# Optimization experiments

Measured on AMD Instinct MI355X. Metric: run time of the kernel, lower is better.

## Reference

```python
import jax, jax.numpy as jnp
import numpy as np

N_NODES = 100000
NUM_FEAT = 64
NUM_CLASS = 40
N_EDGES = 1600000


def setup_inputs() -> dict:
    key = jax.random.key(0)
    k1, k2, k3, k4, k5 = jax.random.split(key, 5)
    x = jax.random.normal(k1, (N_NODES, NUM_FEAT), dtype=jnp.float32)
    index = jax.random.randint(k2, (2, N_EDGES), 0, N_NODES, dtype=jnp.int64)
    # SAGEConv params: lin_l applied to aggregated neighbors (has bias),
    # lin_r applied to root features (no bias) -- PyG convention.
    s = 1.0 / np.sqrt(NUM_FEAT)
    lin_l_w = jax.random.uniform(k3, (NUM_FEAT, NUM_CLASS), dtype=jnp.float32, minval=-s, maxval=s)
    lin_l_b = jnp.zeros((NUM_CLASS,), dtype=jnp.float32)
    lin_r_w = jax.random.uniform(k4, (NUM_FEAT, NUM_CLASS), dtype=jnp.float32, minval=-s, maxval=s)
    return {"x": x, "index": index, "lin_l_w": lin_l_w, "lin_l_b": lin_l_b, "lin_r_w": lin_r_w}


def reference(x, index, lin_l_w, lin_l_b, lin_r_w):
    src, dst = index[0], index[1]
    # Mean aggregation over incoming neighbors: messages flow src -> dst.
    msg = x[src]                                        # [E, F] gather
    agg_sum = jax.ops.segment_sum(msg, dst, num_segments=N_NODES)   # [N, F]
    deg = jax.ops.segment_sum(jnp.ones((index.shape[1],), dtype=x.dtype), dst,
                              num_segments=N_NODES)     # [N]
    agg = agg_sum / jnp.maximum(deg, 1.0)[:, None]      # mean, safe for isolated nodes
    out = agg @ lin_l_w + lin_l_b + x @ lin_r_w         # [N, C]
    return jax.nn.log_softmax(out, axis=1)
```

## Files before the change

kernel.cpp:

```cpp
#include <hip/hip_runtime.h>
#include <hip/hip_fp8.h>
#include <math.h>

constexpr int NODES = 100000;
constexpr int F = 64;
constexpr int C = 40;
constexpr int NPB   = 128;
constexpr int NB    = (NODES + NPB - 1) / NPB;
constexpr int NBPAD = 1024;
constexpr int BCAP  = 2816;
constexpr int TILE  = 4096;
constexpr int NTILES = NODES / 16;
constexpr int MBLK  = (NTILES + 3) / 4;

typedef __attribute__((ext_vector_type(8))) short short8;
typedef __attribute__((ext_vector_type(4))) float floatx4;
typedef __attribute__((ext_vector_type(2))) float floatx2;

__device__ inline unsigned bf16pack2(float a, float b) {
    unsigned ua = __builtin_bit_cast(unsigned, a);
    unsigned ub = __builtin_bit_cast(unsigned, b);
    ua += 0x7FFFu + ((ua >> 16) & 1u);
    ub += 0x7FFFu + ((ub >> 16) & 1u);
    return (ua >> 16) | (ub & 0xFFFF0000u);
}
__device__ inline unsigned short bf16of(float a) {
    unsigned ua = __builtin_bit_cast(unsigned, a);
    ua += 0x7FFFu + ((ua >> 16) & 1u);
    return (unsigned short)(ua >> 16);
}
__device__ inline float bf16tof(unsigned short u) {
    return __builtin_bit_cast(float, (unsigned)u << 16);
}
__device__ inline unsigned char fp8of(float f) {
    __hip_fp8_e4m3 q(f);
    return (unsigned char)q.__x;
}
template <int K>
__device__ inline float fp8byte(unsigned d) {
    __hip_fp8_e4m3 v;
    v.__x = (__hip_fp8_storage_t)((d >> (8 * K)) & 0xFFu);
    return (float)v;
}
template <int HI>
__device__ inline floatx2 fp8pk(unsigned d) {
#if __has_builtin(__builtin_amdgcn_cvt_pk_f32_fp8)
    return __builtin_amdgcn_cvt_pk_f32_fp8((int)d, HI != 0);
#else
    floatx2 r;
    r[0] = fp8byte<HI ? 2 : 0>(d);
    r[1] = fp8byte<HI ? 3 : 1>(d);
    return r;
#endif
}

__global__ __launch_bounds__(256)
void fused_A(const float* __restrict__ x,
             const float* __restrict__ wl,
             const float* __restrict__ bl,
             const float* __restrict__ wr,
             const int* __restrict__ src, const int* __restrict__ dst,
             int* __restrict__ gcursor, int* __restrict__ bbuf, int nedges,
             unsigned char* __restrict__ y8f, unsigned short* __restrict__ z8) {
    __shared__ union {
        struct { int lhist[NB]; int lcur[NB]; } bz;
        struct { unsigned sB[10 * 64 * 4]; float sbl[40]; } mf;
    } sh;

    int t = threadIdx.x;

    if (blockIdx.x < MBLK) {
        if (t < 40) sh.mf.sbl[t] = bl[t];
        for (int s = t; s < 640; s += 256) {
            int region = s >> 6;
            int l      = s & 63;
            int ct = region >> 1, ks = region & 1;
            int col = ct * 16 + (l & 15);
            int fb  = ks * 32 + ((l >> 4) << 3);
            const float* wsrc = (col < 40) ? (wl + col) : (wr + (col - 40));
            unsigned* dstp = &sh.mf.sB[s * 4];
#pragma unroll
            for (int p = 0; p < 4; ++p) {
                float a = wsrc[(fb + 2 * p) * 40];
                float b = wsrc[(fb + 2 * p + 1) * 40];
                dstp[p] = bf16pack2(a, b);
            }
        }
        __syncthreads();

        int lane = t & 63;
        int nt = blockIdx.x * 4 + (t >> 6);
        if (nt >= NTILES) return;

        union U { unsigned u[4]; short8 v; };
        short8 bf[5][2];
#pragma unroll
        for (int ct = 0; ct < 5; ++ct)
#pragma unroll
            for (int ks = 0; ks < 2; ++ks) {
                U tmp;
                const uint4* p =
                    (const uint4*)&sh.mf.sB[((ct * 2 + ks) * 64 + lane) * 4];
                uint4 q = *p;
                tmp.u[0] = q.x; tmp.u[1] = q.y; tmp.u[2] = q.z; tmp.u[3] = q.w;
                bf[ct][ks] = tmp.v;
            }

        floatx4 acc[5];
#pragma unroll
        for (int ct = 0; ct < 5; ++ct) {
            int col = ct * 16 + (lane & 15);
            float bias = (col >= 40) ? sh.mf.sbl[col - 40] : 0.0f;
            acc[ct] = (floatx4){bias, bias, bias, bias};
        }

        int row = nt * 16 + (lane & 15);
        const float4* xp = (const float4*)(x + (size_t)row * F);
        short8 af[2];
#pragma unroll
        for (int ks = 0; ks < 2; ++ks) {
            int kb = ks * 8 + ((lane >> 4) << 1);
            float4 va = xp[kb];
            float4 vb = xp[kb + 1];
            U a;
            a.u[0] = bf16pack2(va.x, va.y);
            a.u[1] = bf16pack2(va.z, va.w);
            a.u[2] = bf16pack2(vb.x, vb.y);
            a.u[3] = bf16pack2(vb.z, vb.w);
            af[ks] = a.v;
        }

#pragma unroll
        for (int ks = 0; ks < 2; ++ks)
#pragma unroll
            for (int ct = 0; ct < 5; ++ct)
                acc[ct] = __builtin_amdgcn_mfma_f32_16x16x32_bf16(
                    af[ks], bf[ct][ks], acc[ct], 0, 0, 0);

#pragma unroll
        for (int ct = 0; ct < 5; ++ct) {
            int col = ct * 16 + (lane & 15);
#pragma unroll
            for (int r = 0; r < 4; ++r) {
                int grow = nt * 16 + ((lane >> 4) << 2) + r;
                if (col < 40) y8f[(size_t)grow * C + col]       = fp8of(acc[ct][r]);
                else          z8[(size_t)grow * C + (col - 40)] = bf16of(acc[ct][r]);
            }
        }
    } else {
        for (int i = t; i < NB; i += 256) sh.bz.lhist[i] = 0;
        __syncthreads();

        int bb = blockIdx.x - MBLK;
        int base = bb * TILE;
        int pk[16], bk[16];
#pragma unroll
        for (int u = 0; u < 16; ++u) {
            int e = base + u * 256 + t;
            bk[u] = -1;
            if (e < nedges) {
                int s = src[e], d = dst[e];
                if ((unsigned)s < (unsigned)NODES && (unsigned)d < (unsigned)NODES) {
                    bk[u] = d >> 7;
                    pk[u] = s | ((d & 127) << 17);
                    atomicAdd(&sh.bz.lhist[bk[u]], 1);
                }
            }
        }
        __syncthreads();
        for (int i = t; i < NB; i += 256) {
            int c = sh.bz.lhist[i];
            sh.bz.lcur[i] = c ? atomicAdd(&gcursor[i], c) : 0;
        }
        __syncthreads();
#pragma unroll
        for (int u = 0; u < 16; ++u) {
            if (bk[u] >= 0) {
                int p = atomicAdd(&sh.bz.lcur[bk[u]], 1);
                if (p < BCAP) bbuf[(size_t)bk[u] * BCAP + p] = pk[u];
            }
        }
    }
}

__global__ __launch_bounds__(256)
void local_sort(const int* __restrict__ bbuf, const int* __restrict__ gcount,
                int* __restrict__ sorted_src, int* __restrict__ off,
                int* __restrict__ deg) {
    __shared__ int lhist[NPB];
    __shared__ int lcur[NPB];
    __shared__ int wred[4];
    __shared__ int w0tot;

    int b = blockIdx.x;
    int t = threadIdx.x;
    int lane = t & 63, wv = t >> 6;

    int part = 0;
    for (int i = t; i < b; i += 256) part += gcount[i];
#pragma unroll
    for (int d = 1; d < 64; d <<= 1) part += __shfl_xor(part, d);
    if (lane == 0) wred[wv] = part;
    if (t < NPB) lhist[t] = 0;
    __syncthreads();
    int ebase = wred[0] + wred[1] + wred[2] + wred[3];

    int cnt = gcount[b];
    if (cnt > BCAP) cnt = BCAP;
    const int* myb = bbuf + (size_t)b * BCAP;

    for (int i = t; i < cnt; i += 256)
        atomicAdd(&lhist[myb[i] >> 17], 1);
    __syncthreads();

    int c = 0, sc = 0;
    if (t < NPB) {
        c = lhist[t];
        sc = c;
#pragma unroll
        for (int d = 1; d < 64; d <<= 1) {
            int o = __shfl_up(sc, d);
            if (lane >= d) sc += o;
        }
    }
    if (t == 63) w0tot = sc;
    __syncthreads();
    if (t >= 64 && t < NPB) sc += w0tot;
    if (t < NPB) {
        int excl = ebase + sc - c;
        lcur[t] = excl;
        int n = b * NPB + t;
        if (n < NODES) { off[n] = excl; deg[n] = c; }
    }
    __syncthreads();

    for (int i = t; i < cnt; i += 256) {
        int pk = myb[i];
        int p = atomicAdd(&lcur[pk >> 17], 1);
        sorted_src[p] = pk & 0x1FFFF;
    }
}

__global__ __launch_bounds__(256)
void aggregate_v4(const unsigned char* __restrict__ y8f,
                  const unsigned short* __restrict__ z8,
                  const int* __restrict__ sorted_src,
                  const int* __restrict__ off,
                  const int* __restrict__ deg,
                  float* __restrict__ out) {
    int t = threadIdx.x;
    int lane = t & 63;
    int n = blockIdx.x * 4 + (t >> 6);
    if (n >= NODES) return;

    int g = lane >> 3;
    int i = lane & 7;
    bool valid = (i < 5);
    int byteoff = (valid ? i : 4) * 8;

    int base = __builtin_amdgcn_readfirstlane(off[n]);
    int cnt  = __builtin_amdgcn_readfirstlane(deg[n]);

    int li = lane < cnt ? lane : (cnt > 0 ? cnt - 1 : 0);
    int idxv = sorted_src[base + li];

    uint4 zv = make_uint4(0u, 0u, 0u, 0u);
    if (valid) zv = *(const uint4*)(z8 + (size_t)n * C + i * 8);

    unsigned d0[8], d1[8];
#pragma unroll
    for (int k = 0; k < 8; ++k) { d0[k] = 0u; d1[k] = 0u; }
#pragma unroll
    for (int k = 0; k < 8; ++k) {
        if (cnt > 8 * k) {
            int s = __shfl(idxv, 8 * k + g);
            const unsigned* p = (const unsigned*)(y8f + (size_t)s * C + byteoff);
            d0[k] = p[0];
            d1[k] = p[1];
        }
    }

    float acc[8] = {0.f, 0.f, 0.f, 0.f, 0.f, 0.f, 0.f, 0.f};
#pragma unroll
    for (int k = 0; k < 8; ++k) {
        if (cnt > 8 * k) {
            float w = (8 * k + g < cnt) ? 1.0f : 0.0f;
            floatx2 l0 = fp8pk<0>(d0[k]);
            floatx2 h0 = fp8pk<1>(d0[k]);
            floatx2 l1 = fp8pk<0>(d1[k]);
            floatx2 h1 = fp8pk<1>(d1[k]);
            acc[0] = fmaf(w, l0[0], acc[0]);
            acc[1] = fmaf(w, l0[1], acc[1]);
            acc[2] = fmaf(w, h0[0], acc[2]);
            acc[3] = fmaf(w, h0[1], acc[3]);
            acc[4] = fmaf(w, l1[0], acc[4]);
            acc[5] = fmaf(w, l1[1], acc[5]);
            acc[6] = fmaf(w, h1[0], acc[6]);
            acc[7] = fmaf(w, h1[1], acc[7]);
        }
    }
    for (int j = 64; j < cnt; j += 8) {
        int e = j + g;
        int ec = e < cnt ? e : cnt - 1;
        int s = sorted_src[base + ec];
        float w = e < cnt ? 1.0f : 0.0f;
        const unsigned* p = (const unsigned*)(y8f + (size_t)s * C + byteoff);
        unsigned a0 = p[0], a1 = p[1];
        floatx2 l0 = fp8pk<0>(a0), h0 = fp8pk<1>(a0);
        floatx2 l1 = fp8pk<0>(a1), h1 = fp8pk<1>(a1);
        acc[0] = fmaf(w, l0[0], acc[0]);
        acc[1] = fmaf(w, l0[1], acc[1]);
        acc[2] = fmaf(w, h0[0], acc[2]);
        acc[3] = fmaf(w, h0[1], acc[3]);
        acc[4] = fmaf(w, l1[0], acc[4]);
        acc[5] = fmaf(w, l1[1], acc[5]);
        acc[6] = fmaf(w, h1[0], acc[6]);
        acc[7] = fmaf(w, h1[1], acc[7]);
    }

#pragma unroll
    for (int m = 8; m <= 32; m <<= 1)
#pragma unroll
        for (int k = 0; k < 8; ++k)
            acc[k] += __shfl_xor(acc[k], m);

    float inv = 1.0f / (float)(cnt > 0 ? cnt : 1);

    float o[8];
    if (valid) {
        unsigned zu[4] = {zv.x, zv.y, zv.z, zv.w};
#pragma unroll
        for (int k = 0; k < 4; ++k) {
            o[2 * k]     = bf16tof((unsigned short)(zu[k] & 0xFFFFu))
                         + acc[2 * k] * inv;
            o[2 * k + 1] = bf16tof((unsigned short)(zu[k] >> 16))
                         + acc[2 * k + 1] * inv;
        }
    } else {
#pragma unroll
        for (int k = 0; k < 8; ++k) o[k] = -1e30f;
    }

    float mv = -1e30f;
    if (valid)
#pragma unroll
        for (int k = 0; k < 8; ++k) mv = fmaxf(mv, o[k]);
#pragma unroll
    for (int m = 1; m <= 4; m <<= 1) mv = fmaxf(mv, __shfl_xor(mv, m));

    float ev = 0.0f;
    if (valid)
#pragma unroll
        for (int k = 0; k < 8; ++k) ev += __expf(o[k] - mv);
#pragma unroll
    for (int m = 1; m <= 4; m <<= 1) ev += __shfl_xor(ev, m);
    float lse = mv + __logf(ev);

    if (valid && g == 0) {
        float4 o0 = make_float4(o[0] - lse, o[1] - lse, o[2] - lse, o[3] - lse);
        float4 o1 = make_float4(o[4] - lse, o[5] - lse, o[6] - lse, o[7] - lse);
        float4* op = (float4*)(out + (size_t)n * C + i * 8);
        op[0] = o0;
        op[1] = o1;
    }
}

__global__ __launch_bounds__(256)
void scatter_kernel(const float* __restrict__ x, const int* __restrict__ src,
                    const int* __restrict__ dst, float* __restrict__ aggsum,
                    float* __restrict__ deg, int nedges) {
    int lane = threadIdx.x & 63;
    int e = blockIdx.x * 4 + (threadIdx.x >> 6);
    if (e >= nedges) return;
    int s = src[e], d = dst[e];
    if ((unsigned)s >= (unsigned)NODES || (unsigned)d >= (unsigned)NODES) return;
    atomicAdd(&aggsum[(size_t)d * F + lane], x[(size_t)s * F + lane]);
    if (lane == 0) atomicAdd(&deg[d], 1.0f);
}

__global__ __launch_bounds__(256)
void meanify_kernel(float* __restrict__ aggsum, const float* __restrict__ deg) {
    int lane = threadIdx.x & 63;
    int n = blockIdx.x * 4 + (threadIdx.x >> 6);
    if (n >= NODES) return;
    aggsum[(size_t)n * F + lane] *= 1.0f / fmaxf(deg[n], 1.0f);
}

__global__ __launch_bounds__(256)
void node_kernel(const float* __restrict__ x, const float* __restrict__ aggmean,
                 const float* __restrict__ wl, const float* __restrict__ bl,
                 const float* __restrict__ wr, float* __restrict__ out) {
    __shared__ alignas(16) float sWl[F * C];
    __shared__ alignas(16) float sWr[F * C];
    __shared__ alignas(16) float sb[C];
    for (int i = threadIdx.x; i < F * C; i += 256) { sWl[i] = wl[i]; sWr[i] = wr[i]; }
    if (threadIdx.x < C) sb[threadIdx.x] = bl[threadIdx.x];
    __syncthreads();
    int n = blockIdx.x * 256 + threadIdx.x;
    if (n >= NODES) return;
    float4 acc[10];
    const float4* sb4 = (const float4*)sb;
#pragma unroll
    for (int q = 0; q < 10; ++q) acc[q] = sb4[q];
    const float4* xr  = (const float4*)(x       + (size_t)n * F);
    const float4* ar  = (const float4*)(aggmean + (size_t)n * F);
    const float4* wl4 = (const float4*)sWl;
    const float4* wr4 = (const float4*)sWr;
    for (int f4 = 0; f4 < F / 4; ++f4) {
        float4 xv = xr[f4], av = ar[f4];
        float xs[4]  = {xv.x, xv.y, xv.z, xv.w};
        float as_[4] = {av.x, av.y, av.z, av.w};
#pragma unroll
        for (int jj = 0; jj < 4; ++jj) {
            int f = f4 * 4 + jj;
#pragma unroll
            for (int q = 0; q < 10; ++q) {
                float4 wlv = wl4[f * 10 + q], wrv = wr4[f * 10 + q];
                acc[q].x = fmaf(as_[jj], wlv.x, fmaf(xs[jj], wrv.x, acc[q].x));
                acc[q].y = fmaf(as_[jj], wlv.y, fmaf(xs[jj], wrv.y, acc[q].y));
                acc[q].z = fmaf(as_[jj], wlv.z, fmaf(xs[jj], wrv.z, acc[q].z));
                acc[q].w = fmaf(as_[jj], wlv.w, fmaf(xs[jj], wrv.w, acc[q].w));
            }
        }
    }
    float m = -1e30f;
#pragma unroll
    for (int q = 0; q < 10; ++q)
        m = fmaxf(m, fmaxf(fmaxf(acc[q].x, acc[q].y), fmaxf(acc[q].z, acc[q].w)));
    float ssum = 0.0f;
#pragma unroll
    for (int q = 0; q < 10; ++q)
        ssum += __expf(acc[q].x - m) + __expf(acc[q].y - m) +
                __expf(acc[q].z - m) + __expf(acc[q].w - m);
    float lse = m + __logf(ssum);
    float4* op = (float4*)(out + (size_t)n * C);
#pragma unroll
    for (int q = 0; q < 10; ++q) {
        float4 v;
        v.x = acc[q].x - lse; v.y = acc[q].y - lse;
        v.z = acc[q].z - lse; v.w = acc[q].w - lse;
        op[q] = v;
    }
}

extern "C" void kernel_launch(void* const* d_in, const int* in_sizes, int n_in,
                              void* d_out, int out_size, void* d_ws, size_t ws_size,
                              hipStream_t stream) {
    const float* x     = (const float*)d_in[0];
    const int*   index = (const int*)d_in[1];
    const float* wl    = (const float*)d_in[2];
    const float* bl    = (const float*)d_in[3];
    const float* wr    = (const float*)d_in[4];
    float* out = (float*)d_out;

    int nedges = in_sizes[1] / 2;
    const int* src = index;
    const int* dst = index + nedges;

    size_t need = (size_t)NODES * C * 3
                + ((size_t)NB * BCAP + (size_t)nedges + 2 * (size_t)NODES + NBPAD) * 4;

    if (ws_size >= need) {
        unsigned short* z8 = (unsigned short*)d_ws;
        unsigned char* y8f = (unsigned char*)(z8 + (size_t)NODES * C);
        int* bbuf       = (int*)(y8f + (size_t)NODES * C);
        int* sorted_src = bbuf + (size_t)NB * BCAP;
        int* off        = sorted_src + nedges;
        int* deg        = off + NODES;
        int* gcursor    = deg + NODES;

        hipMemsetAsync(gcursor, 0, NBPAD * sizeof(int), stream);

        int bblocks = (nedges + TILE - 1) / TILE;
        fused_A<<<MBLK + bblocks, 256, 0, stream>>>(
            x, wl, bl, wr, src, dst, gcursor, bbuf, nedges, y8f, z8);
        local_sort<<<NB, 256, 0, stream>>>(bbuf, gcursor, sorted_src, off, deg);
        aggregate_v4<<<(NODES + 3) / 4, 256, 0, stream>>>(
            y8f, z8, sorted_src, off, deg, out);
    } else {
        float* aggsum = (float*)d_ws;
        float* deg    = aggsum + (size_t)NODES * F;
        hipMemsetAsync(d_ws, 0,
                       ((size_t)NODES * F + NODES) * sizeof(float), stream);
        scatter_kernel<<<(nedges + 3) / 4, 256, 0, stream>>>(
            x, src, dst, aggsum, deg, nedges);
        meanify_kernel<<<(NODES + 3) / 4, 256, 0, stream>>>(aggsum, deg);
        node_kernel<<<(NODES + 255) / 256, 256, 0, stream>>>(
            x, aggsum, wl, bl, wr, out);
    }
}
```

Measured before the change: 166.8 us.

## Pad fp8 rows to 64 bytes, reorder fused blocks, cache buckets in LDS

After: 191.5 us. 1.15x slower.

```diff
diff --git a/kernel.cpp b/kernel.cpp
--- a/kernel.cpp
+++ b/kernel.cpp
@@ -5,13 +5,13 @@
 constexpr int NODES = 100000;
 constexpr int F = 64;
 constexpr int C = 40;
+constexpr int YSTR = 64;
 constexpr int NPB   = 128;
 constexpr int NB    = (NODES + NPB - 1) / NPB;
 constexpr int NBPAD = 1024;
 constexpr int BCAP  = 2816;
-constexpr int TILE  = 4096;
+constexpr int TILE  = 16384;
 constexpr int NTILES = NODES / 16;
-constexpr int MBLK  = (NTILES + 3) / 4;
 
 typedef __attribute__((ext_vector_type(8))) short short8;
 typedef __attribute__((ext_vector_type(4))) float floatx4;
@@ -61,6 +61,7 @@
              const float* __restrict__ wr,
              const int* __restrict__ src, const int* __restrict__ dst,
              int* __restrict__ gcursor, int* __restrict__ bbuf, int nedges,
+             int bblocks,
              unsigned char* __restrict__ y8f, unsigned short* __restrict__ z8) {
     __shared__ union {
         struct { int lhist[NB]; int lcur[NB]; } bz;
@@ -69,7 +70,35 @@
 
     int t = threadIdx.x;
 
-    if (blockIdx.x < MBLK) {
+    if ((int)blockIdx.x < bblocks) {
+        for (int i = t; i < NB; i += 256) sh.bz.lhist[i] = 0;
+        __syncthreads();
+
+        int base = blockIdx.x * TILE;
+        int end  = base + TILE;
+        if (end > nedges) end = nedges;
+
+        for (int e = base + t; e < end; e += 256) {
+            int s = src[e], d = dst[e];
+            if ((unsigned)s < (unsigned)NODES && (unsigned)d < (unsigned)NODES)
+                atomicAdd(&sh.bz.lhist[d >> 7], 1);
+        }
+        __syncthreads();
+        for (int i = t; i < NB; i += 256) {
+            int c = sh.bz.lhist[i];
+            sh.bz.lcur[i] = c ? atomicAdd(&gcursor[i], c) : 0;
+        }
+        __syncthreads();
+        for (int e = base + t; e < end; e += 256) {
+            int s = src[e], d = dst[e];
+            if ((unsigned)s < (unsigned)NODES && (unsigned)d < (unsigned)NODES) {
+                int b = d >> 7;
+                int p = atomicAdd(&sh.bz.lcur[b], 1);
+                if (p < BCAP)
+                    bbuf[(size_t)b * BCAP + p] = s | ((d & 127) << 17);
+            }
+        }
+    } else {
         if (t < 40) sh.mf.sbl[t] = bl[t];
         for (int s = t; s < 640; s += 256) {
             int region = s >> 6;
@@ -89,7 +118,7 @@
         __syncthreads();
 
         int lane = t & 63;
-        int nt = blockIdx.x * 4 + (t >> 6);
+        int nt = (blockIdx.x - bblocks) * 4 + (t >> 6);
         if (nt >= NTILES) return;
 
         union U { unsigned u[4]; short8 v; };
@@ -143,41 +172,10 @@
 #pragma unroll
             for (int r = 0; r < 4; ++r) {
                 int grow = nt * 16 + ((lane >> 4) << 2) + r;
-                if (col < 40) y8f[(size_t)grow * C + col]       = fp8of(acc[ct][r]);
-                else          z8[(size_t)grow * C + (col - 40)] = bf16of(acc[ct][r]);
-            }
-        }
-    } else {
-        for (int i = t; i < NB; i += 256) sh.bz.lhist[i] = 0;
-        __syncthreads();
-
-        int bb = blockIdx.x - MBLK;
-        int base = bb * TILE;
-        int pk[16], bk[16];
-#pragma unroll
-        for (int u = 0; u < 16; ++u) {
-            int e = base + u * 256 + t;
-            bk[u] = -1;
-            if (e < nedges) {
-                int s = src[e], d = dst[e];
-                if ((unsigned)s < (unsigned)NODES && (unsigned)d < (unsigned)NODES) {
-                    bk[u] = d >> 7;
-                    pk[u] = s | ((d & 127) << 17);
-                    atomicAdd(&sh.bz.lhist[bk[u]], 1);
-                }
-            }
-        }
-        __syncthreads();
-        for (int i = t; i < NB; i += 256) {
-            int c = sh.bz.lhist[i];
-            sh.bz.lcur[i] = c ? atomicAdd(&gcursor[i], c) : 0;
-        }
-        __syncthreads();
-#pragma unroll
-        for (int u = 0; u < 16; ++u) {
-            if (bk[u] >= 0) {
-                int p = atomicAdd(&sh.bz.lcur[bk[u]], 1);
-                if (p < BCAP) bbuf[(size_t)bk[u] * BCAP + p] = pk[u];
+                if (col < 40)
+                    y8f[(size_t)grow * YSTR + col] = fp8of(acc[ct][r]);
+                else
+                    z8[(size_t)grow * C + (col - 40)] = bf16of(acc[ct][r]);
             }
         }
     }
@@ -191,6 +189,7 @@
     __shared__ int lcur[NPB];
     __shared__ int wred[4];
     __shared__ int w0tot;
+    __shared__ int ebuf[BCAP];
 
     int b = blockIdx.x;
     int t = threadIdx.x;
@@ -209,8 +208,11 @@
     if (cnt > BCAP) cnt = BCAP;
     const int* myb = bbuf + (size_t)b * BCAP;
 
-    for (int i = t; i < cnt; i += 256)
-        atomicAdd(&lhist[myb[i] >> 17], 1);
+    for (int i = t; i < cnt; i += 256) {
+        int pk = myb[i];
+        ebuf[i] = pk;
+        atomicAdd(&lhist[pk >> 17], 1);
+    }
     __syncthreads();
 
     int c = 0, sc = 0;
@@ -235,14 +237,14 @@
     __syncthreads();
 
     for (int i = t; i < cnt; i += 256) {
-        int pk = myb[i];
+        int pk = ebuf[i];
         int p = atomicAdd(&lcur[pk >> 17], 1);
         sorted_src[p] = pk & 0x1FFFF;
     }
 }
 
 __global__ __launch_bounds__(256)
-void aggregate_v4(const unsigned char* __restrict__ y8f,
+void aggregate_v5(const unsigned char* __restrict__ y8f,
                   const unsigned short* __restrict__ z8,
                   const int* __restrict__ sorted_src,
                   const int* __restrict__ off,
@@ -274,55 +276,49 @@
     for (int k = 0; k < 8; ++k) {
         if (cnt > 8 * k) {
             int s = __shfl(idxv, 8 * k + g);
-            const unsigned* p = (const unsigned*)(y8f + (size_t)s * C + byteoff);
+            const unsigned* p =
+                (const unsigned*)(y8f + ((size_t)s << 6) + byteoff);
             d0[k] = p[0];
             d1[k] = p[1];
         }
     }
 
-    float acc[8] = {0.f, 0.f, 0.f, 0.f, 0.f, 0.f, 0.f, 0.f};
+    floatx2 acc2[4];
+#pragma unroll
+    for (int k = 0; k < 4; ++k) acc2[k] = (floatx2){0.f, 0.f};
 #pragma unroll
     for (int k = 0; k < 8; ++k) {
         if (cnt > 8 * k) {
-            float w = (8 * k + g < cnt) ? 1.0f : 0.0f;
-            floatx2 l0 = fp8pk<0>(d0[k]);
-            floatx2 h0 = fp8pk<1>(d0[k]);
-            floatx2 l1 = fp8pk<0>(d1[k]);
-            floatx2 h1 = fp8pk<1>(d1[k]);
-            acc[0] = fmaf(w, l0[0], acc[0]);
-            acc[1] = fmaf(w, l0[1], acc[1]);
-            acc[2] = fmaf(w, h0[0], acc[2]);
-            acc[3] = fmaf(w, h0[1], acc[3]);
-            acc[4] = fmaf(w, l1[0], acc[4]);
-            acc[5] = fmaf(w, l1[1], acc[5]);
-            acc[6] = fmaf(w, h1[0], acc[6]);
-            acc[7] = fmaf(w, h1[1], acc[7]);
+            bool live = (8 * k + g < cnt);
+            unsigned a0 = live ? d0[k] : 0u;
+            unsigned a1 = live ? d1[k] : 0u;
+            acc2[0] += fp8pk<0>(a0);
+            acc2[1] += fp8pk<1>(a0);
+            acc2[2] += fp8pk<0>(a1);
+            acc2[3] += fp8pk<1>(a1);
         }
     }
     for (int j = 64; j < cnt; j += 8) {
         int e = j + g;
         int ec = e < cnt ? e : cnt - 1;
         int s = sorted_src[base + ec];
-        float w = e < cnt ? 1.0f : 0.0f;
-        const unsigned* p = (const unsigned*)(y8f + (size_t)s * C + byteoff);
-        unsigned a0 = p[0], a1 = p[1];
-        floatx2 l0 = fp8pk<0>(a0), h0 = fp8pk<1>(a0);
-        floatx2 l1 = fp8pk<0>(a1), h1 = fp8pk<1>(a1);
-        acc[0] = fmaf(w, l0[0], acc[0]);
-        acc[1] = fmaf(w, l0[1], acc[1]);
-        acc[2] = fmaf(w, h0[0], acc[2]);
-        acc[3] = fmaf(w, h0[1], acc[3]);
-        acc[4] = fmaf(w, l1[0], acc[4]);
-        acc[5] = fmaf(w, l1[1], acc[5]);
-        acc[6] = fmaf(w, h1[0], acc[6]);
-        acc[7] = fmaf(w, h1[1], acc[7]);
+        bool live = (e < cnt);
+        const unsigned* p = (const unsigned*)(y8f + ((size_t)s << 6) + byteoff);
+        unsigned a0 = live ? p[0] : 0u;
+        unsigned a1 = live ? p[1] : 0u;
+        acc2[0] += fp8pk<0>(a0);
+        acc2[1] += fp8pk<1>(a0);
+        acc2[2] += fp8pk<0>(a1);
+        acc2[3] += fp8pk<1>(a1);
     }
 
 #pragma unroll
     for (int m = 8; m <= 32; m <<= 1)
 #pragma unroll
-        for (int k = 0; k < 8; ++k)
-            acc[k] += __shfl_xor(acc[k], m);
+        for (int k = 0; k < 4; ++k) {
+            acc2[k][0] += __shfl_xor(acc2[k][0], m);
+            acc2[k][1] += __shfl_xor(acc2[k][1], m);
+        }
 
     float inv = 1.0f / (float)(cnt > 0 ? cnt : 1);
 
@@ -332,9 +328,9 @@
 #pragma unroll
         for (int k = 0; k < 4; ++k) {
             o[2 * k]     = bf16tof((unsigned short)(zu[k] & 0xFFFFu))
-                         + acc[2 * k] * inv;
+                         + acc2[k][0] * inv;
             o[2 * k + 1] = bf16tof((unsigned short)(zu[k] >> 16))
-                         + acc[2 * k + 1] * inv;
+                         + acc2[k][1] * inv;
         }
     } else {
 #pragma unroll
@@ -457,13 +453,13 @@
     const int* src = index;
     const int* dst = index + nedges;
 
-    size_t need = (size_t)NODES * C * 3
+    size_t need = (size_t)NODES * C * 2 + (size_t)NODES * YSTR
                 + ((size_t)NB * BCAP + (size_t)nedges + 2 * (size_t)NODES + NBPAD) * 4;
 
     if (ws_size >= need) {
         unsigned short* z8 = (unsigned short*)d_ws;
         unsigned char* y8f = (unsigned char*)(z8 + (size_t)NODES * C);
-        int* bbuf       = (int*)(y8f + (size_t)NODES * C);
+        int* bbuf       = (int*)(y8f + (size_t)NODES * YSTR);
         int* sorted_src = bbuf + (size_t)NB * BCAP;
         int* off        = sorted_src + nedges;
         int* deg        = off + NODES;
@@ -472,10 +468,11 @@
         hipMemsetAsync(gcursor, 0, NBPAD * sizeof(int), stream);
 
         int bblocks = (nedges + TILE - 1) / TILE;
-        fused_A<<<MBLK + bblocks, 256, 0, stream>>>(
-            x, wl, bl, wr, src, dst, gcursor, bbuf, nedges, y8f, z8);
+        int mblocks = (NTILES + 3) / 4;
+        fused_A<<<bblocks + mblocks, 256, 0, stream>>>(
+            x, wl, bl, wr, src, dst, gcursor, bbuf, nedges, bblocks, y8f, z8);
         local_sort<<<NB, 256, 0, stream>>>(bbuf, gcursor, sorted_src, off, deg);
-        aggregate_v4<<<(NODES + 3) / 4, 256, 0, stream>>>(
+        aggregate_v5<<<(NODES + 3) / 4, 256, 0, stream>>>(
             y8f, z8, sorted_src, off, deg, out);
     } else {
         float* aggsum = (float*)d_ws;
```
